# Kernel optimization log

Hardware: AMD Instinct MI355X
Metric: run time of the kernel (lower is better)

Reference implementation:

```python
import jax, jax.numpy as jnp
import numpy as np

B, L, D = 4, 256, 2048
LE, DE = 2048, 1024
H = 16
HD = D // H  # 128
ROPE_BASE = 10000.0


def apply_rope(q):
    # q: [B, H, L, HD]; rotate interleaved pairs along seq axis L (torchtune-style)
    half = HD // 2
    inv_freq = 1.0 / (ROPE_BASE ** (jnp.arange(0, HD, 2, dtype=jnp.float32) / HD))  # [half]
    pos = jnp.arange(L, dtype=jnp.float32)
    ang = pos[:, None] * inv_freq[None, :]           # [L, half]
    cos = jnp.cos(ang)[None, None, :, :]             # [1,1,L,half]
    sin = jnp.sin(ang)[None, None, :, :]
    qr = q.reshape(B, H, L, half, 2)
    q1, q2 = qr[..., 0], qr[..., 1]
    out = jnp.stack([q1 * cos - q2 * sin, q1 * sin + q2 * cos], axis=-1)
    return out.reshape(B, H, L, HD)


def setup_inputs() -> dict:
    key = jax.random.key(0)
    ks = jax.random.split(key, 7)
    s_d = 1.0 / np.sqrt(D)
    s_e = 1.0 / np.sqrt(DE)
    return {
        "x": jax.random.normal(ks[0], (B, L, D), jnp.float32),
        "encoder_inputs": jax.random.normal(ks[1], (B, LE, DE), jnp.float32),
        "Wq": jax.random.normal(ks[2], (D, D), jnp.float32) * s_d,
        "bq": jnp.zeros((D,), jnp.float32),
        "Wk": jax.random.normal(ks[3], (DE, D), jnp.float32) * s_e,
        "bk": jnp.zeros((D,), jnp.float32),
        "Wv": jax.random.normal(ks[4], (DE, D), jnp.float32) * s_e,
        "bv": jnp.zeros((D,), jnp.float32),
        "Wo": jax.random.normal(ks[5], (D, D), jnp.float32) * s_d,
        "bo": jnp.zeros((D,), jnp.float32),
    }


def reference(x, encoder_inputs, Wq, bq, Wk, bk, Wv, bv, Wo, bo):
    q = (x @ Wq + bq).reshape(B, L, H, HD).transpose(0, 2, 1, 3)              # [B,H,L,HD]
    k = (encoder_inputs @ Wk + bk).reshape(B, LE, H, HD).transpose(0, 2, 1, 3)  # [B,H,Le,HD]
    v = (encoder_inputs @ Wv + bv).reshape(B, LE, H, HD).transpose(0, 2, 1, 3)
    q = apply_rope(q)
    scale = 1.0 / jnp.sqrt(jnp.float32(HD))
    scores = jnp.einsum("bhld,bhmd->bhlm", q, k) * scale                      # [B,H,L,Le]
    attn = jax.nn.softmax(scores, axis=-1)
    ctx = jnp.einsum("bhlm,bhmd->bhld", attn, v)                              # [B,H,L,HD]
    ctx = ctx.transpose(0, 2, 1, 3).reshape(B, L, D)
    return ctx @ Wo + bo
```

## Files before the change

kernel.cpp:

```cpp
#include <hip/hip_runtime.h>


#define B_ 4
#define L_ 256
#define D_ 2048
#define LE_ 2048
#define DE_ 1024
#define H_ 16
#define HD_ 128

using f32x4  = __attribute__((ext_vector_type(4))) float;
using bf16x8 = __attribute__((ext_vector_type(8))) short;

__device__ __forceinline__ unsigned short f2bf(float f) {
    union { float f; unsigned int u; } v; v.f = f;
    unsigned int r = v.u + 0x7fffu + ((v.u >> 16) & 1u);
    return (unsigned short)(r >> 16);
}
__device__ __forceinline__ float b2f(unsigned short h) {
    union { unsigned int u; float f; } v; v.u = ((unsigned int)h) << 16;
    return v.f;
}

__device__ __forceinline__ void load_lds16(const void* g, void* l) {
    __builtin_amdgcn_global_load_lds((const __attribute__((address_space(1))) void*)g,
                                     (__attribute__((address_space(3))) void*)l, 16, 0, 0);
}

__global__ void cast_f32_bf16(const float* __restrict__ in, unsigned short* __restrict__ out, int n) {
    int i = (blockIdx.x * 256 + threadIdx.x) * 4;
    if (i < n) {
        float4 v = *(const float4*)(in + i);
        ushort4 o;
        o.x = f2bf(v.x); o.y = f2bf(v.y); o.z = f2bf(v.z); o.w = f2bf(v.w);
        *(ushort4*)(out + i) = o;
    }
}

__global__ void transpose_f32_bf16(const float* __restrict__ in, unsigned short* __restrict__ out,
                                   int R, int C) {
    __shared__ float t[32][33];
    int r0 = blockIdx.y * 32, c0 = blockIdx.x * 32;
    int tx = threadIdx.x, ty = threadIdx.y;
    #pragma unroll
    for (int i = 0; i < 32; i += 8) t[ty + i][tx] = in[(long)(r0 + ty + i) * C + c0 + tx];
    __syncthreads();
    #pragma unroll
    for (int i = 0; i < 32; i += 8) out[(long)(c0 + ty + i) * R + r0 + tx] = f2bf(t[tx][ty + i]);
}

__global__ void transpose_bf16_batched(const unsigned short* __restrict__ in,
                                       unsigned short* __restrict__ out, int R, int C) {
    __shared__ unsigned short t[32][33];
    long zo = (long)blockIdx.z * R * C;
    int r0 = blockIdx.y * 32, c0 = blockIdx.x * 32;
    int tx = threadIdx.x, ty = threadIdx.y;
    #pragma unroll
    for (int i = 0; i < 32; i += 8) t[ty + i][tx] = in[zo + (long)(r0 + ty + i) * C + c0 + tx];
    __syncthreads();
    #pragma unroll
    for (int i = 0; i < 32; i += 8) out[zo + (long)(c0 + ty + i) * R + r0 + tx] = t[tx][ty + i];
}

__global__ void combine_q_rope(const float* __restrict__ P, const float* __restrict__ bq,
                               unsigned short* __restrict__ Q) {
    int gid = blockIdx.x * 256 + threadIdx.x;
    int p = gid & 63;
    int h = (gid >> 6) & 15;
    int m = gid >> 10;
    int n = h * 128 + 2 * p;
    long i0 = (long)m * 2048 + n;
    float q1 = bq[n], q2 = bq[n + 1];
    #pragma unroll
    for (int pt = 0; pt < 4; pt++) {
        float2 a = *(const float2*)(P + (long)pt * 2097152 + i0);
        q1 += a.x; q2 += a.y;
    }
    int l = m & 255, b = m >> 8;
    float inv = powf(10000.0f, -(float)p * (1.0f / 64.0f));
    float s, c;
    sincosf((float)l * inv, &s, &c);
    const float sc = 0.08838834764831845f;
    long qi = (((long)(b * 16 + h) * 256 + l) << 7) + 2 * p;
    ushort2 o;
    o.x = f2bf((q1 * c - q2 * s) * sc);
    o.y = f2bf((q1 * s + q2 * c) * sc);
    *(ushort2*)(Q + qi) = o;
}

__global__ void combine_pv(const float* __restrict__ P, unsigned short* __restrict__ ctx) {
    int gid = blockIdx.x * 256 + threadIdx.x;
    long e = (long)gid * 4;
    float4 a = *(const float4*)(P + e);
    #pragma unroll
    for (int pt = 1; pt < 4; pt++) {
        float4 b = *(const float4*)(P + (long)pt * 2097152 + e);
        a.x += b.x; a.y += b.y; a.z += b.z; a.w += b.w;
    }
    int bh = (int)(e >> 15);
    int m  = (int)((e >> 7) & 255);
    int d  = (int)(e & 127);
    int bb = bh >> 4, h = bh & 15;
    ushort4 o;
    o.x = f2bf(a.x); o.y = f2bf(a.y); o.z = f2bf(a.z); o.w = f2bf(a.w);
    *(ushort4*)(ctx + ((long)(bb * 256 + m)) * 2048 + h * 128 + d) = o;
}

__global__ void combine_o(const float* __restrict__ P, const float* __restrict__ bo,
                          float* __restrict__ out) {
    int gid = blockIdx.x * 256 + threadIdx.x;
    long e = (long)gid * 4;
    int n = (int)(e & 2047);
    float4 r = *(const float4*)(bo + n);
    #pragma unroll
    for (int pt = 0; pt < 4; pt++) {
        float4 a = *(const float4*)(P + (long)pt * 2097152 + e);
        r.x += a.x; r.y += a.y; r.z += a.z; r.w += a.w;
    }
    *(float4*)(out + e) = r;
}

__launch_bounds__(256)
__global__ void softmax_rows(unsigned short* __restrict__ S) {
    long row = blockIdx.x;
    unsigned short* p = S + row * 2048;
    int t = threadIdx.x, w = t >> 6, lane = t & 63;
    bf16x8 raw = *(const bf16x8*)(p + t * 8);
    float v[8];
    float mx = -1e30f;
    #pragma unroll
    for (int i = 0; i < 8; i++) { v[i] = b2f((unsigned short)raw[i]); mx = fmaxf(mx, v[i]); }
    #pragma unroll
    for (int o = 32; o; o >>= 1) mx = fmaxf(mx, __shfl_xor(mx, o));
    __shared__ float redm[4], reds[4];
    if (lane == 0) redm[w] = mx;
    __syncthreads();
    mx = fmaxf(fmaxf(redm[0], redm[1]), fmaxf(redm[2], redm[3]));
    float sum = 0.f;
    #pragma unroll
    for (int i = 0; i < 8; i++) { v[i] = __expf(v[i] - mx); sum += v[i]; }
    #pragma unroll
    for (int o = 32; o; o >>= 1) sum += __shfl_xor(sum, o);
    if (lane == 0) reds[w] = sum;
    __syncthreads();
    sum = reds[0] + reds[1] + reds[2] + reds[3];
    float r = 1.0f / sum;
    bf16x8 res;
    #pragma unroll
    for (int i = 0; i < 8; i++) res[i] = (short)f2bf(v[i] * r);
    *(bf16x8*)(p + t * 8) = res;
}

template <int EPI>
__launch_bounds__(256)
__global__ void gemm_bt(const unsigned short* __restrict__ A, const unsigned short* __restrict__ Bt,
                        const float* __restrict__ biasA, const float* __restrict__ biasB,
                        void* __restrict__ outA, void* __restrict__ outB,
                        int M, int N, int K, int lda, int ldb,
                        long strideA, long strideB, int zdiv, int nsplit) {
    __shared__ __align__(16) unsigned short smem[24576];
    const int z = blockIdx.z;
    int s = 0, bh = z;
    if constexpr (EPI == 4) { s = z / zdiv; bh = z - s * zdiv; }
    const unsigned short* Ab = A + (long)bh * strideA + (long)s * K;
    const unsigned short* Bb = Bt + (long)bh * strideB + (long)s * K;
    const int m0 = blockIdx.y * 128, n0 = blockIdx.x * 128;
    const int tid = threadIdx.x;
    const int w = tid >> 6, lane = tid & 63;
    const int quad = lane >> 4, l16 = lane & 15;
    const int wr = w >> 1, wc = w & 1;
    const int srow = lane >> 2;
    const int scol = (lane & 3) * 8;

    f32x4 acc[4][4] = {};

    auto stage = [&](int k0, int p) {
        unsigned short* As = smem + p * 8192;
        unsigned short* Bs = As + 4096;
        #pragma unroll
        for (int q = 0; q < 2; q++) {
            int ci = q * 4 + w;
            int row = ci * 16 + srow;
            load_lds16(Ab + (long)(m0 + row) * lda + k0 + scol, (void*)(As + ci * 512));
            load_lds16(Bb + (long)(n0 + row) * ldb + k0 + scol, (void*)(Bs + ci * 512));
        }
    };

    const int nk = K >> 5;
    stage(0, 0);
    stage(32, 1);
    int p = 0;
    for (int i = 0; i < nk; i++) {
        if (i + 1 < nk) asm volatile("s_waitcnt vmcnt(4)" ::: "memory");
        else            asm volatile("s_waitcnt vmcnt(0)" ::: "memory");
        __builtin_amdgcn_s_barrier();
        if (i + 2 < nk) {
            int pn = p + 2; if (pn >= 3) pn -= 3;
            stage((i + 2) << 5, pn);
        }
        const unsigned short* As = smem + p * 8192;
        const unsigned short* Bs = As + 4096;
        bf16x8 af[4], bfr[4];
        #pragma unroll
        for (int ii = 0; ii < 4; ii++) {
            int r = wr * 64 + ii * 16 + l16;
            af[ii] = *(const bf16x8*)(As + r * 32 + quad * 8);
        }
        #pragma unroll
        for (int j = 0; j < 4; j++) {
            int r = wc * 64 + j * 16 + l16;
            bfr[j] = *(const bf16x8*)(Bs + r * 32 + quad * 8);
        }
        #pragma unroll
        for (int ii = 0; ii < 4; ii++)
            #pragma unroll
            for (int j = 0; j < 4; j++)
                acc[ii][j] = __builtin_amdgcn_mfma_f32_16x16x32_bf16(af[ii], bfr[j], acc[ii][j], 0, 0, 0);
        if (++p >= 3) p -= 3;
    }
    __syncthreads();

    if constexpr (EPI == 1 || EPI == 2) {
        const bool second = (EPI == 1) && (n0 >= nsplit);
        const float* bias = second ? biasB : biasA;
        const int n0e = second ? n0 - nsplit : n0;
        unsigned short* dst = (unsigned short*)(second ? outB : outA);
        #pragma unroll
        for (int pp = 0; pp < 2; pp++) {
            if (wr == pp) {
                #pragma unroll
                for (int i = 0; i < 4; i++)
                    #pragma unroll
                    for (int j = 0; j < 4; j++)
                        #pragma unroll
                        for (int r = 0; r < 4; r++) {
                            int ml = i * 16 + quad * 4 + r;
                            int n  = wc * 64 + j * 16 + l16;
                            float v = acc[i][j][r];
                            if (bias) v += bias[n0e + n];
                            smem[ml * 136 + n] = f2bf(v);
                        }
            }
            __syncthreads();
            #pragma unroll
            for (int pass = 0; pass < 4; pass++) {
                int row = pass * 16 + (tid >> 4);
                int seg = tid & 15;
                bf16x8 val = *(const bf16x8*)(smem + row * 136 + seg * 8);
                int m = m0 + pp * 64 + row;
                if constexpr (EPI == 1) {
                    int h = n0e >> 7;
                    int b = m >> 11, mrow = m & 2047;
                    long idx = (((long)(b * 16 + h)) << 11) + mrow;
                    *(bf16x8*)(dst + (idx << 7) + seg * 8) = val;
                } else {
                    *(bf16x8*)((unsigned short*)outA + (long)z * M * N + (long)m * N + n0 + seg * 8) = val;
                }
            }
            __syncthreads();
        }
    } else {
        float* smf = (float*)smem;
        long zo = ((long)s * zdiv + bh) * (long)M * N;
        #pragma unroll
        for (int q4 = 0; q4 < 4; q4++) {
            if (wr == (q4 >> 1)) {
                #pragma unroll
                for (int ii = 0; ii < 2; ii++) {
                    int i = (q4 & 1) * 2 + ii;
                    #pragma unroll
                    for (int j = 0; j < 4; j++)
                        #pragma unroll
                        for (int r = 0; r < 4; r++) {
                            int ml = ii * 16 + quad * 4 + r;
                            int n  = wc * 64 + j * 16 + l16;
                            smf[ml * 132 + n] = acc[i][j][r];
                        }
                }
            }
            __syncthreads();
            #pragma unroll
            for (int pass = 0; pass < 4; pass++) {
                int row = pass * 8 + (tid >> 5);
                int seg = tid & 31;
                float4 val = *(const float4*)(smf + row * 132 + seg * 4);
                int m = m0 + q4 * 32 + row;
                *(float4*)((float*)outA + zo + (long)m * N + n0 + seg * 4) = val;
            }
            __syncthreads();
        }
    }
}

extern "C" void kernel_launch(void* const* d_in, const int* in_sizes, int n_in,
                              void* d_out, int out_size, void* d_ws, size_t ws_size,
                              hipStream_t stream) {
    const float* x   = (const float*)d_in[0];
    const float* enc = (const float*)d_in[1];
    const float* Wq  = (const float*)d_in[2];
    const float* bq  = (const float*)d_in[3];
    const float* Wk  = (const float*)d_in[4];
    const float* bk  = (const float*)d_in[5];
    const float* Wv  = (const float*)d_in[6];
    const float* bv  = (const float*)d_in[7];
    const float* Wo  = (const float*)d_in[8];
    const float* bo  = (const float*)d_in[9];
    float* out = (float*)d_out;

    char* ws = (char*)d_ws;
    const size_t MB = 1024 * 1024;
    unsigned short* x_bf   = (unsigned short*)(ws + 0 * MB);
    unsigned short* enc_bf = (unsigned short*)(ws + 4 * MB);
    unsigned short* WqT    = (unsigned short*)(ws + 20 * MB);
    unsigned short* WkvT   = (unsigned short*)(ws + 28 * MB);
    unsigned short* V_bf   = (unsigned short*)(ws + 36 * MB);
    unsigned short* K_bf   = (unsigned short*)(ws + 68 * MB);
    unsigned short* WoT    = (unsigned short*)(ws + 100 * MB);
    unsigned short* Q_bf   = (unsigned short*)(ws + 108 * MB);
    unsigned short* Vt     = (unsigned short*)(ws + 112 * MB);
    unsigned short* S_bf   = (unsigned short*)(ws + 0 * MB);
    float*          Pq     = (float*)(ws + 36 * MB);
    float*          Ppv    = (float*)(ws + 68 * MB);
    float*          Po     = (float*)(ws + 0 * MB);
    unsigned short* ctx_bf = (unsigned short*)(ws + 108 * MB);

    dim3 tb(32, 8);

    cast_f32_bf16<<<2048, 256, 0, stream>>>(x, x_bf, 2097152);
    cast_f32_bf16<<<8192, 256, 0, stream>>>(enc, enc_bf, 8388608);

    transpose_f32_bf16<<<dim3(64, 64), tb, 0, stream>>>(Wq, WqT, 2048, 2048);
    transpose_f32_bf16<<<dim3(64, 32), tb, 0, stream>>>(Wk, WkvT, 1024, 2048);
    transpose_f32_bf16<<<dim3(64, 32), tb, 0, stream>>>(Wv, WkvT + 2048 * 1024, 1024, 2048);
    transpose_f32_bf16<<<dim3(64, 64), tb, 0, stream>>>(Wo, WoT, 2048, 2048);

    gemm_bt<4><<<dim3(16, 8, 4), 256, 0, stream>>>(x_bf, WqT, nullptr, nullptr, Pq, nullptr,
                                                   1024, 2048, 512, 2048, 2048, 0, 0, 1, 0);
    combine_q_rope<<<4096, 256, 0, stream>>>(Pq, bq, Q_bf);

    gemm_bt<1><<<dim3(32, 64, 1), 256, 0, stream>>>(enc_bf, WkvT, bk, bv, K_bf, V_bf,
                                                    8192, 4096, 1024, 1024, 1024, 0, 0, 1, 2048);

    transpose_bf16_batched<<<dim3(4, 64, 64), tb, 0, stream>>>(V_bf, Vt, 2048, 128);

    gemm_bt<2><<<dim3(16, 2, 64), 256, 0, stream>>>(Q_bf, K_bf, nullptr, nullptr, S_bf, nullptr,
                                                    256, 2048, 128, 128, 128,
                                                    256 * 128, 2048 * 128, 1, 0);
    softmax_rows<<<16384, 256, 0, stream>>>(S_bf);

    gemm_bt<4><<<dim3(1, 2, 256), 256, 0, stream>>>(S_bf, Vt, nullptr, nullptr, Ppv, nullptr,
                                                    256, 128, 512, 2048, 2048,
                                                    256 * 2048, 128 * 2048, 64, 0);
    combine_pv<<<2048, 256, 0, stream>>>(Ppv, ctx_bf);

    gemm_bt<4><<<dim3(16, 8, 4), 256, 0, stream>>>(ctx_bf, WoT, nullptr, nullptr, Po, nullptr,
                                                   1024, 2048, 512, 2048, 2048, 0, 0, 1, 0);
    combine_o<<<2048, 256, 0, stream>>>(Po, bo, out);
}
```

Measured before the change: 406.0 us.

## Fuse prep kernels, write V transposed in GEMM epilogue, use double-buffered pipeline

```diff
diff --git a/kernel.cpp b/kernel.cpp
--- a/kernel.cpp
+++ b/kernel.cpp
@@ -27,39 +27,42 @@
                                      (__attribute__((address_space(3))) void*)l, 16, 0, 0);
 }
 
-__global__ void cast_f32_bf16(const float* __restrict__ in, unsigned short* __restrict__ out, int n) {
-    int i = (blockIdx.x * 256 + threadIdx.x) * 4;
-    if (i < n) {
-        float4 v = *(const float4*)(in + i);
-        ushort4 o;
-        o.x = f2bf(v.x); o.y = f2bf(v.y); o.z = f2bf(v.z); o.w = f2bf(v.w);
-        *(ushort4*)(out + i) = o;
-    }
-}
-
-__global__ void transpose_f32_bf16(const float* __restrict__ in, unsigned short* __restrict__ out,
-                                   int R, int C) {
+__global__ void cast_all(const float* __restrict__ x, const float* __restrict__ enc,
+                         unsigned short* __restrict__ x_bf, unsigned short* __restrict__ enc_bf) {
+    long i = (long)(blockIdx.x * 256 + threadIdx.x) * 4;
+    const float* in;
+    unsigned short* out;
+    if (i < 2097152) { in = x + i; out = x_bf + i; }
+    else             { in = enc + (i - 2097152); out = enc_bf + (i - 2097152); }
+    float4 v = *(const float4*)in;
+    ushort4 o;
+    o.x = f2bf(v.x); o.y = f2bf(v.y); o.z = f2bf(v.z); o.w = f2bf(v.w);
+    *(ushort4*)out = o;
+}
+
+__global__ void transpose_weights(const float* __restrict__ Wq, const float* __restrict__ Wk,
+                                  const float* __restrict__ Wv, const float* __restrict__ Wo,
+                                  unsigned short* __restrict__ WqT, unsigned short* __restrict__ WkvT,
+                                  unsigned short* __restrict__ WoT) {
     __shared__ float t[32][33];
+    const float* in;
+    unsigned short* out;
+    int R;
+    const int C = 2048;
+    switch (blockIdx.z) {
+        case 0:  in = Wq; out = WqT;                R = 2048; break;
+        case 1:  in = Wk; out = WkvT;               R = 1024; break;
+        case 2:  in = Wv; out = WkvT + 2048 * 1024; R = 1024; break;
+        default: in = Wo; out = WoT;                R = 2048; break;
+    }
     int r0 = blockIdx.y * 32, c0 = blockIdx.x * 32;
+    if (r0 >= R) return;
     int tx = threadIdx.x, ty = threadIdx.y;
     #pragma unroll
     for (int i = 0; i < 32; i += 8) t[ty + i][tx] = in[(long)(r0 + ty + i) * C + c0 + tx];
     __syncthreads();
     #pragma unroll
     for (int i = 0; i < 32; i += 8) out[(long)(c0 + ty + i) * R + r0 + tx] = f2bf(t[tx][ty + i]);
-}
-
-__global__ void transpose_bf16_batched(const unsigned short* __restrict__ in,
-                                       unsigned short* __restrict__ out, int R, int C) {
-    __shared__ unsigned short t[32][33];
-    long zo = (long)blockIdx.z * R * C;
-    int r0 = blockIdx.y * 32, c0 = blockIdx.x * 32;
-    int tx = threadIdx.x, ty = threadIdx.y;
-    #pragma unroll
-    for (int i = 0; i < 32; i += 8) t[ty + i][tx] = in[zo + (long)(r0 + ty + i) * C + c0 + tx];
-    __syncthreads();
-    #pragma unroll
-    for (int i = 0; i < 32; i += 8) out[zo + (long)(c0 + ty + i) * R + r0 + tx] = t[tx][ty + i];
 }
 
 __global__ void combine_q_rope(const float* __restrict__ P, const float* __restrict__ bq,
@@ -158,7 +161,7 @@
                         void* __restrict__ outA, void* __restrict__ outB,
                         int M, int N, int K, int lda, int ldb,
                         long strideA, long strideB, int zdiv, int nsplit) {
-    __shared__ __align__(16) unsigned short smem[24576];
+    __shared__ __align__(16) unsigned short smem[16384];
     const int z = blockIdx.z;
     int s = 0, bh = z;
     if constexpr (EPI == 4) { s = z / zdiv; bh = z - s * zdiv; }
@@ -188,17 +191,10 @@
 
     const int nk = K >> 5;
     stage(0, 0);
-    stage(32, 1);
-    int p = 0;
     for (int i = 0; i < nk; i++) {
-        if (i + 1 < nk) asm volatile("s_waitcnt vmcnt(4)" ::: "memory");
-        else            asm volatile("s_waitcnt vmcnt(0)" ::: "memory");
-        __builtin_amdgcn_s_barrier();
-        if (i + 2 < nk) {
-            int pn = p + 2; if (pn >= 3) pn -= 3;
-            stage((i + 2) << 5, pn);
-        }
-        const unsigned short* As = smem + p * 8192;
+        __syncthreads();
+        if (i + 1 < nk) stage((i + 1) << 5, (i + 1) & 1);
+        const unsigned short* As = smem + (i & 1) * 8192;
         const unsigned short* Bs = As + 4096;
         bf16x8 af[4], bfr[4];
         #pragma unroll
@@ -216,15 +212,72 @@
             #pragma unroll
             for (int j = 0; j < 4; j++)
                 acc[ii][j] = __builtin_amdgcn_mfma_f32_16x16x32_bf16(af[ii], bfr[j], acc[ii][j], 0, 0, 0);
-        if (++p >= 3) p -= 3;
     }
     __syncthreads();
 
-    if constexpr (EPI == 1 || EPI == 2) {
-        const bool second = (EPI == 1) && (n0 >= nsplit);
-        const float* bias = second ? biasB : biasA;
-        const int n0e = second ? n0 - nsplit : n0;
-        unsigned short* dst = (unsigned short*)(second ? outB : outA);
+    if constexpr (EPI == 1) {
+        const int b = m0 >> 11;
+        const int le0 = m0 & 2047;
+        if (n0 < nsplit) {
+            const int h = n0 >> 7;
+            unsigned short* dst = (unsigned short*)outA + ((((long)(b * 16 + h)) << 11) << 7);
+            #pragma unroll
+            for (int pp = 0; pp < 2; pp++) {
+                if (wr == pp) {
+                    #pragma unroll
+                    for (int i = 0; i < 4; i++)
+                        #pragma unroll
+                        for (int j = 0; j < 4; j++)
+                            #pragma unroll
+                            for (int r = 0; r < 4; r++) {
+                                int ml = i * 16 + quad * 4 + r;
+                                int n  = wc * 64 + j * 16 + l16;
+                                smem[ml * 136 + n] = f2bf(acc[i][j][r] + biasA[n0 + n]);
+                            }
+                }
+                __syncthreads();
+                #pragma unroll
+                for (int pass = 0; pass < 4; pass++) {
+                    int row = pass * 16 + (tid >> 4);
+                    int seg = tid & 15;
+                    bf16x8 val = *(const bf16x8*)(smem + row * 136 + seg * 8);
+                    long le = le0 + pp * 64 + row;
+                    *(bf16x8*)(dst + (le << 7) + seg * 8) = val;
+                }
+                __syncthreads();
+            }
+        } else {
+            const int n0e = n0 - nsplit;
+            const int h = n0e >> 7;
+            unsigned short* vbase = (unsigned short*)outB + ((long)(b * 16 + h)) * (128 * 2048);
+            #pragma unroll
+            for (int pp = 0; pp < 2; pp++) {
+                if (wr == pp) {
+                    #pragma unroll
+                    for (int i = 0; i < 4; i++)
+                        #pragma unroll
+                        for (int j = 0; j < 4; j++) {
+                            int d = wc * 64 + j * 16 + l16;
+                            float bvd = biasB[n0e + d];
+                            #pragma unroll
+                            for (int r = 0; r < 4; r++) {
+                                int ml = i * 16 + quad * 4 + r;
+                                smem[d * 72 + ml] = f2bf(acc[i][j][r] + bvd);
+                            }
+                        }
+                }
+                __syncthreads();
+                #pragma unroll
+                for (int pass = 0; pass < 4; pass++) {
+                    int d = pass * 32 + (tid >> 3);
+                    int c = tid & 7;
+                    bf16x8 val = *(const bf16x8*)(smem + d * 72 + c * 8);
+                    *(bf16x8*)(vbase + (long)d * 2048 + le0 + pp * 64 + c * 8) = val;
+                }
+                __syncthreads();
+            }
+        }
+    } else if constexpr (EPI == 2) {
         #pragma unroll
         for (int pp = 0; pp < 2; pp++) {
             if (wr == pp) {
@@ -236,9 +289,7 @@
                         for (int r = 0; r < 4; r++) {
                             int ml = i * 16 + quad * 4 + r;
                             int n  = wc * 64 + j * 16 + l16;
-                            float v = acc[i][j][r];
-                            if (bias) v += bias[n0e + n];
-                            smem[ml * 136 + n] = f2bf(v);
+                            smem[ml * 136 + n] = f2bf(acc[i][j][r]);
                         }
             }
             __syncthreads();
@@ -248,14 +299,7 @@
                 int seg = tid & 15;
                 bf16x8 val = *(const bf16x8*)(smem + row * 136 + seg * 8);
                 int m = m0 + pp * 64 + row;
-                if constexpr (EPI == 1) {
-                    int h = n0e >> 7;
-                    int b = m >> 11, mrow = m & 2047;
-                    long idx = (((long)(b * 16 + h)) << 11) + mrow;
-                    *(bf16x8*)(dst + (idx << 7) + seg * 8) = val;
-                } else {
-                    *(bf16x8*)((unsigned short*)outA + (long)z * M * N + (long)m * N + n0 + seg * 8) = val;
-                }
+                *(bf16x8*)((unsigned short*)outA + (long)z * M * N + (long)m * N + n0 + seg * 8) = val;
             }
             __syncthreads();
         }
@@ -313,7 +357,6 @@
     unsigned short* enc_bf = (unsigned short*)(ws + 4 * MB);
     unsigned short* WqT    = (unsigned short*)(ws + 20 * MB);
     unsigned short* WkvT   = (unsigned short*)(ws + 28 * MB);
-    unsigned short* V_bf   = (unsigned short*)(ws + 36 * MB);
     unsigned short* K_bf   = (unsigned short*)(ws + 68 * MB);
     unsigned short* WoT    = (unsigned short*)(ws + 100 * MB);
     unsigned short* Q_bf   = (unsigned short*)(ws + 108 * MB);
@@ -324,24 +367,16 @@
     float*          Po     = (float*)(ws + 0 * MB);
     unsigned short* ctx_bf = (unsigned short*)(ws + 108 * MB);
 
-    dim3 tb(32, 8);
-
-    cast_f32_bf16<<<2048, 256, 0, stream>>>(x, x_bf, 2097152);
-    cast_f32_bf16<<<8192, 256, 0, stream>>>(enc, enc_bf, 8388608);
-
-    transpose_f32_bf16<<<dim3(64, 64), tb, 0, stream>>>(Wq, WqT, 2048, 2048);
-    transpose_f32_bf16<<<dim3(64, 32), tb, 0, stream>>>(Wk, WkvT, 1024, 2048);
-    transpose_f32_bf16<<<dim3(64, 32), tb, 0, stream>>>(Wv, WkvT + 2048 * 1024, 1024, 2048);
-    transpose_f32_bf16<<<dim3(64, 64), tb, 0, stream>>>(Wo, WoT, 2048, 2048);
+    cast_all<<<10240, 256, 0, stream>>>(x, enc, x_bf, enc_bf);
+
+    transpose_weights<<<dim3(64, 64, 4), dim3(32, 8), 0, stream>>>(Wq, Wk, Wv, Wo, WqT, WkvT, WoT);
 
     gemm_bt<4><<<dim3(16, 8, 4), 256, 0, stream>>>(x_bf, WqT, nullptr, nullptr, Pq, nullptr,
                                                    1024, 2048, 512, 2048, 2048, 0, 0, 1, 0);
     combine_q_rope<<<4096, 256, 0, stream>>>(Pq, bq, Q_bf);
 
-    gemm_bt<1><<<dim3(32, 64, 1), 256, 0, stream>>>(enc_bf, WkvT, bk, bv, K_bf, V_bf,
+    gemm_bt<1><<<dim3(32, 64, 1), 256, 0, stream>>>(enc_bf, WkvT, bk, bv, K_bf, Vt,
                                                     8192, 4096, 1024, 1024, 1024, 0, 0, 1, 2048);
-
-    transpose_bf16_batched<<<dim3(4, 64, 64), tb, 0, stream>>>(V_bf, Vt, 2048, 128);
 
     gemm_bt<2><<<dim3(16, 2, 64), 256, 0, stream>>>(Q_bf, K_bf, nullptr, nullptr, S_bf, nullptr,
                                                     256, 2048, 128, 128, 128,
```

Measured after the change: 362.9 us. 1.12x faster.
